# Optimization experiments

Hardware: AMD Instinct MI355X
Metric: run time of the kernel (lower is better)

## Reference

```python
import jax, jax.numpy as jnp
import numpy as np

C = 512      # input/value channels
DK = 64      # key/query channels (C // 8, SAGAN convention)
N = 4096     # flattened spatial positions (64x64)


def setup_inputs() -> dict:
    key = jax.random.key(0)
    k1, k2, k3, k4 = jax.random.split(key, 4)
    x = jax.random.normal(k1, (C, N), dtype=jnp.float32)
    # 1x1 conv projections == linear maps over the channel dim
    Wk = jax.random.normal(k2, (DK, C), dtype=jnp.float32) * (1.0 / np.sqrt(C))
    Wq = jax.random.normal(k3, (DK, C), dtype=jnp.float32) * (1.0 / np.sqrt(C))
    Wv = jax.random.normal(k4, (C, C), dtype=jnp.float32) * (1.0 / np.sqrt(C))
    return {"x": x, "Wk": Wk, "Wq": Wq, "Wv": Wv}


def reference(x, Wk, Wq, Wv):
    # conv 1x1 projections: [dk, N] / [dk, N] / [C, N]
    kx = Wk @ x
    qx = Wq @ x
    vx = Wv @ x
    # alpha_{i,j} = softmax_j( f(x_i)^T g(x_j) )  -> [N, N]
    scores = jnp.einsum('di,dj->ij', kx, qx)
    attn = jax.nn.softmax(scores, axis=-1)
    # o_i = sum_j alpha_{i,j} h(x_j)  -> [N, C]
    out = attn @ vx.T
    return out
```

## Files before the change

kernel.cpp:

```cpp
#include <hip/hip_runtime.h>
#include <hip/hip_bf16.h>

typedef __bf16 bf16x8 __attribute__((ext_vector_type(8)));
typedef float f32x4 __attribute__((ext_vector_type(4)));
typedef unsigned int u32x4 __attribute__((ext_vector_type(4)));

#define MFMA16(a, b, c) __builtin_amdgcn_mfma_f32_16x16x32_bf16((a), (b), (c), 0, 0, 0)
#define DEVI static __device__ __forceinline__

DEVI unsigned short f2bf(float f) {
  union { float f; unsigned u; } x; x.f = f;
  unsigned r = x.u + 0x7fffu + ((x.u >> 16) & 1u);
  return (unsigned short)(r >> 16);
}
DEVI float bf2f(unsigned short h) {
  union { unsigned u; float f; } x; x.u = ((unsigned)h) << 16;
  return x.f;
}
DEVI bf16x8 ld16(const void* p) {
  u32x4 t = *reinterpret_cast<const u32x4*>(p);
  return __builtin_bit_cast(bf16x8, t);
}

__global__ __launch_bounds__(256) void xsplit_kernel(const float* __restrict__ x,
    unsigned short* __restrict__ xThi, unsigned short* __restrict__ xTlo) {
  __shared__ unsigned short hs[64][72];
  __shared__ unsigned short ls[64][72];
  const int c0 = blockIdx.x * 64, j0 = blockIdx.y * 64;
  const int t = threadIdx.x;
  {
    const int cr = t >> 2, jc = (t & 3) * 16;
    const float4* s4 = reinterpret_cast<const float4*>(x + (c0 + cr) * 4096 + j0 + jc);
#pragma unroll
    for (int q = 0; q < 4; ++q) {
      float4 v = s4[q];
      float vv[4] = {v.x, v.y, v.z, v.w};
#pragma unroll
      for (int e = 0; e < 4; ++e) {
        unsigned short h = f2bf(vv[e]);
        hs[cr][jc + q * 4 + e] = h;
        ls[cr][jc + q * 4 + e] = f2bf(vv[e] - bf2f(h));
      }
    }
  }
  __syncthreads();
  {
    const int jr = t >> 2, cc = (t & 3) * 16;
    unsigned short hb[16] __attribute__((aligned(16)));
    unsigned short lb[16] __attribute__((aligned(16)));
#pragma unroll
    for (int u = 0; u < 16; ++u) { hb[u] = hs[cc + u][jr]; lb[u] = ls[cc + u][jr]; }
    unsigned short* dh = xThi + (j0 + jr) * 512 + c0 + cc;
    unsigned short* dl = xTlo + (j0 + jr) * 512 + c0 + cc;
    reinterpret_cast<u32x4*>(dh)[0] = reinterpret_cast<const u32x4*>(hb)[0];
    reinterpret_cast<u32x4*>(dh)[1] = reinterpret_cast<const u32x4*>(hb)[1];
    reinterpret_cast<u32x4*>(dl)[0] = reinterpret_cast<const u32x4*>(lb)[0];
    reinterpret_cast<u32x4*>(dl)[1] = reinterpret_cast<const u32x4*>(lb)[1];
  }
}

__global__ __launch_bounds__(256) void wsplit_all_kernel(
    const float* __restrict__ Wk, const float* __restrict__ Wq, const float* __restrict__ Wv,
    unsigned short* __restrict__ Wkhi, unsigned short* __restrict__ Wklo,
    unsigned short* __restrict__ Wqhi, unsigned short* __restrict__ Wqlo,
    unsigned short* __restrict__ Wvhi, unsigned short* __restrict__ Wvlo) {
  const int nk = 64 * 512 / 4, nv = 512 * 512 / 4;
  int i = blockIdx.x * 256 + threadIdx.x;
  const float* in; unsigned short* hi; unsigned short* lo; int idx;
  if (i < nk)            { in = Wk; hi = Wkhi; lo = Wklo; idx = i; }
  else if (i < 2 * nk)   { in = Wq; hi = Wqhi; lo = Wqlo; idx = i - nk; }
  else if (i < 2 * nk + nv) { in = Wv; hi = Wvhi; lo = Wvlo; idx = i - 2 * nk; }
  else return;
  float4 v = reinterpret_cast<const float4*>(in)[idx];
  float vv[4] = {v.x, v.y, v.z, v.w};
  unsigned short hb[4] __attribute__((aligned(8)));
  unsigned short lb[4] __attribute__((aligned(8)));
#pragma unroll
  for (int e = 0; e < 4; ++e) { hb[e] = f2bf(vv[e]); lb[e] = f2bf(vv[e] - bf2f(hb[e])); }
  reinterpret_cast<uint2*>(hi)[idx] = *reinterpret_cast<const uint2*>(hb);
  reinterpret_cast<uint2*>(lo)[idx] = *reinterpret_cast<const uint2*>(lb);
}

__global__ __launch_bounds__(256) void kqproj_kernel(
    const unsigned short* __restrict__ Wkhi, const unsigned short* __restrict__ Wklo,
    const unsigned short* __restrict__ Wqhi, const unsigned short* __restrict__ Wqlo,
    const unsigned short* __restrict__ xThi, const unsigned short* __restrict__ xTlo,
    unsigned short* __restrict__ kxThi, unsigned short* __restrict__ kxTlo,
    unsigned short* __restrict__ qxThi, unsigned short* __restrict__ qxTlo) {
  const int mb = blockIdx.y;
  const int w = threadIdx.x >> 6, lane = threadIdx.x & 63;
  const int li = lane & 15, g = lane >> 4;
  const int j0 = blockIdx.x * 64 + w * 16;
  const unsigned short* Whi = (mb < 4 ? Wkhi : Wqhi) + ((mb & 3) * 16 + li) * 512 + g * 8;
  const unsigned short* Wlo = (mb < 4 ? Wklo : Wqlo) + ((mb & 3) * 16 + li) * 512 + g * 8;
  const unsigned short* Xh = xThi + (j0 + li) * 512 + g * 8;
  const unsigned short* Xl = xTlo + (j0 + li) * 512 + g * 8;
  f32x4 acc = f32x4{0.f, 0.f, 0.f, 0.f};
  for (int kf = 0; kf < 16; ++kf) {
    const int o = kf * 32;
    bf16x8 ah = ld16(Whi + o), al = ld16(Wlo + o);
    bf16x8 bh = ld16(Xh + o), bl = ld16(Xl + o);
    acc = MFMA16(ah, bh, acc);
    acc = MFMA16(ah, bl, acc);
    acc = MFMA16(al, bh, acc);
  }
  unsigned short hv[4] __attribute__((aligned(8))), lv[4] __attribute__((aligned(8)));
#pragma unroll
  for (int r = 0; r < 4; ++r) {
    hv[r] = f2bf(acc[r]);
    lv[r] = f2bf(acc[r] - bf2f(hv[r]));
  }
  unsigned short* oh = (mb < 4 ? kxThi : qxThi) + (j0 + li) * 64 + (mb & 3) * 16 + g * 4;
  unsigned short* ol = (mb < 4 ? kxTlo : qxTlo) + (j0 + li) * 64 + (mb & 3) * 16 + g * 4;
  *reinterpret_cast<uint2*>(oh) = *reinterpret_cast<const uint2*>(hv);
  *reinterpret_cast<uint2*>(ol) = *reinterpret_cast<const uint2*>(lv);
}

__global__ __launch_bounds__(256) void vproj_kernel(
    const unsigned short* __restrict__ Wvhi, const unsigned short* __restrict__ Wvlo,
    const unsigned short* __restrict__ xThi, const unsigned short* __restrict__ xTlo,
    unsigned short* __restrict__ vbf) {
  const int w = threadIdx.x >> 6, lane = threadIdx.x & 63;
  const int li = lane & 15, g = lane >> 4;
  const int j0 = blockIdx.x * 64 + (w >> 1) * 32;
  const int c0 = blockIdx.y * 64 + (w & 1) * 32;
  f32x4 acc[2][2];
#pragma unroll
  for (int mf = 0; mf < 2; ++mf)
#pragma unroll
    for (int nf = 0; nf < 2; ++nf) acc[mf][nf] = f32x4{0.f, 0.f, 0.f, 0.f};
  for (int kf = 0; kf < 16; ++kf) {
    const int kk = kf * 32 + g * 8;
    bf16x8 ah[2], al[2], bh[2], bl[2];
#pragma unroll
    for (int mf = 0; mf < 2; ++mf) {
      ah[mf] = ld16(xThi + (j0 + mf * 16 + li) * 512 + kk);
      al[mf] = ld16(xTlo + (j0 + mf * 16 + li) * 512 + kk);
    }
#pragma unroll
    for (int nf = 0; nf < 2; ++nf) {
      bh[nf] = ld16(Wvhi + (c0 + nf * 16 + li) * 512 + kk);
      bl[nf] = ld16(Wvlo + (c0 + nf * 16 + li) * 512 + kk);
    }
#pragma unroll
    for (int mf = 0; mf < 2; ++mf)
#pragma unroll
      for (int nf = 0; nf < 2; ++nf) {
        acc[mf][nf] = MFMA16(ah[mf], bh[nf], acc[mf][nf]);
        acc[mf][nf] = MFMA16(ah[mf], bl[nf], acc[mf][nf]);
        acc[mf][nf] = MFMA16(al[mf], bh[nf], acc[mf][nf]);
      }
  }
#pragma unroll
  for (int mf = 0; mf < 2; ++mf)
#pragma unroll
    for (int nf = 0; nf < 2; ++nf) {
      unsigned short hv[4] __attribute__((aligned(8)));
#pragma unroll
      for (int r = 0; r < 4; ++r) hv[r] = f2bf(acc[mf][nf][r]);
      *reinterpret_cast<uint2*>(vbf + (size_t)(c0 + nf * 16 + li) * 4096 + j0 + mf * 16 + g * 4) =
          *reinterpret_cast<const uint2*>(hv);
    }
}

__global__ __launch_bounds__(256, 2) void attn_kernel(
    const unsigned short* __restrict__ kxThi, const unsigned short* __restrict__ kxTlo,
    const unsigned short* __restrict__ qxThi, const unsigned short* __restrict__ qxTlo,
    const unsigned short* __restrict__ vbf,
    unsigned short* __restrict__ pacc, float* __restrict__ pml, int split) {
  __shared__ __align__(16) unsigned short QLh[4096];
  __shared__ __align__(16) unsigned short QLl[4096];
  __shared__ __align__(16) unsigned short PL[4096];
  __shared__ __align__(16) float smax[64][4];
  __shared__ __align__(16) float ssum[64][4];
  const int jchunk = 4096 / split;
  const int s = blockIdx.x % split;
  const int i0 = (blockIdx.x / split) * 64;
  const int jbase = s * jchunk;
  const int w = threadIdx.x >> 6, lane = threadIdx.x & 63;
  const int li = lane & 15, g = lane >> 4;
  const float L2E = 1.4426950408889634f;
  char* qlh = reinterpret_cast<char*>(QLh);
  char* qll = reinterpret_cast<char*>(QLl);
  char* plb = reinterpret_cast<char*>(PL);

  {
    const int qi = threadIdx.x >> 2;
#pragma unroll
    for (int cc = 0; cc < 2; ++cc) {
      const int ch = (threadIdx.x & 3) + cc * 4;
      const int src = (i0 + qi) * 64 + ch * 8;
      const int dst = (qi * 128 + ch * 16) ^ ((qi & 7) << 4);
      *reinterpret_cast<u32x4*>(qlh + dst) = *reinterpret_cast<const u32x4*>(kxThi + src);
      *reinterpret_cast<u32x4*>(qll + dst) = *reinterpret_cast<const u32x4*>(kxTlo + src);
    }
  }
  f32x4 acc[8][4];
#pragma unroll
  for (int cf = 0; cf < 8; ++cf)
#pragma unroll
    for (int f = 0; f < 4; ++f) acc[cf][f] = f32x4{0.f, 0.f, 0.f, 0.f};
  float m_run[4] = {-3.0e38f, -3.0e38f, -3.0e38f, -3.0e38f};
  float l_run[4] = {0.f, 0.f, 0.f, 0.f};
  __syncthreads();

  for (int jj = 0; jj < jchunk; jj += 64) {
    const int j0 = jbase + jj;
    f32x4 sc[4];
#pragma unroll
    for (int f = 0; f < 4; ++f) sc[f] = f32x4{0.f, 0.f, 0.f, 0.f};
    {
      const unsigned short* ah_p = qxThi + (j0 + w * 16 + li) * 64 + g * 8;
      const unsigned short* al_p = qxTlo + (j0 + w * 16 + li) * 64 + g * 8;
#pragma unroll
      for (int kf = 0; kf < 2; ++kf) {
        bf16x8 ah = ld16(ah_p + kf * 32);
        bf16x8 al = ld16(al_p + kf * 32);
#pragma unroll
        for (int f = 0; f < 4; ++f) {
          const int qb = ((f * 16 + li) * 128 + kf * 64 + g * 16) ^ ((li & 7) << 4);
          bf16x8 qh = ld16(qlh + qb);
          bf16x8 ql = ld16(qll + qb);
          sc[f] = MFMA16(ah, qh, sc[f]);
          sc[f] = MFMA16(ah, ql, sc[f]);
          sc[f] = MFMA16(al, qh, sc[f]);
        }
      }
    }
    {
      float pm[4];
#pragma unroll
      for (int f = 0; f < 4; ++f) {
        float t = fmaxf(fmaxf(sc[f][0], sc[f][1]), fmaxf(sc[f][2], sc[f][3]));
        t = fmaxf(t, __shfl_xor(t, 16));
        t = fmaxf(t, __shfl_xor(t, 32));
        pm[f] = t;
      }
      if (lane < 16) {
#pragma unroll
        for (int f = 0; f < 4; ++f) smax[f * 16 + li][w] = pm[f];
      }
    }
    __syncthreads();
    float m_new[4], fac[4];
#pragma unroll
    for (int f = 0; f < 4; ++f) {
      const f32x4 sm = *reinterpret_cast<const f32x4*>(&smax[f * 16 + li][0]);
      m_new[f] = fmaxf(m_run[f], fmaxf(fmaxf(sm[0], sm[1]), fmaxf(sm[2], sm[3])));
      fac[f] = exp2f((m_run[f] - m_new[f]) * L2E);
      m_run[f] = m_new[f];
    }
#pragma unroll
    for (int f = 0; f < 4; ++f) {
      float p[4];
#pragma unroll
      for (int r = 0; r < 4; ++r) p[r] = exp2f((sc[f][r] - m_new[f]) * L2E);
      float ps = (p[0] + p[1]) + (p[2] + p[3]);
      ps += __shfl_xor(ps, 16);
      ps += __shfl_xor(ps, 32);
      if (lane < 16) ssum[f * 16 + li][w] = ps;
      unsigned short pv[4] __attribute__((aligned(8)));
#pragma unroll
      for (int r = 0; r < 4; ++r) pv[r] = f2bf(p[r]);
      const int pb = ((f * 16 + li) * 128 + w * 32 + g * 8) ^ ((li & 7) << 4);
      *reinterpret_cast<uint2*>(plb + pb) = *reinterpret_cast<const uint2*>(pv);
    }
    __syncthreads();
#pragma unroll
    for (int f = 0; f < 4; ++f) {
      const f32x4 ss = *reinterpret_cast<const f32x4*>(&ssum[f * 16 + li][0]);
      l_run[f] = l_run[f] * fac[f] + ((ss[0] + ss[1]) + (ss[2] + ss[3]));
    }
#pragma unroll
    for (int cf = 0; cf < 8; ++cf)
#pragma unroll
      for (int f = 0; f < 4; ++f) {
#pragma unroll
        for (int r = 0; r < 4; ++r) acc[cf][f][r] *= fac[f];
      }
    bf16x8 bp[4][2];
#pragma unroll
    for (int f = 0; f < 4; ++f)
#pragma unroll
      for (int kf = 0; kf < 2; ++kf) {
        const int rb = ((f * 16 + li) * 128 + kf * 64 + g * 16) ^ ((li & 7) << 4);
        bp[f][kf] = ld16(plb + rb);
      }
#pragma unroll
    for (int cf = 0; cf < 8; ++cf) {
      const unsigned short* vp = vbf + (size_t)(w * 128 + cf * 16 + li) * 4096 + j0 + g * 8;
      bf16x8 a0 = ld16(vp);
      bf16x8 a1 = ld16(vp + 32);
#pragma unroll
      for (int f = 0; f < 4; ++f) {
        acc[cf][f] = MFMA16(a0, bp[f][0], acc[cf][f]);
        acc[cf][f] = MFMA16(a1, bp[f][1], acc[cf][f]);
      }
    }
  }
#pragma unroll
  for (int cf = 0; cf < 8; ++cf)
#pragma unroll
    for (int f = 0; f < 4; ++f) {
      unsigned short hv[4] __attribute__((aligned(8)));
#pragma unroll
      for (int r = 0; r < 4; ++r) hv[r] = f2bf(acc[cf][f][r]);
      unsigned short* dp = pacc + ((size_t)(s * 4096 + i0 + f * 16 + li)) * 512 + w * 128 + cf * 16 + g * 4;
      *reinterpret_cast<uint2*>(dp) = *reinterpret_cast<const uint2*>(hv);
    }
  if (w == 0 && lane < 16) {
#pragma unroll
    for (int f = 0; f < 4; ++f) {
      pml[((size_t)(s * 4096 + i0 + f * 16 + li)) * 2] = m_run[f];
      pml[((size_t)(s * 4096 + i0 + f * 16 + li)) * 2 + 1] = l_run[f];
    }
  }
}

__global__ __launch_bounds__(256) void combine_kernel(
    const unsigned short* __restrict__ pacc, const float* __restrict__ pml,
    float* __restrict__ out, int split) {
  const int t = blockIdx.x * 256 + threadIdx.x;
  const int i = t >> 6, c8 = (t & 63) << 3;
  const float L2E = 1.4426950408889634f;
  float M = -3.0e38f;
  for (int ss = 0; ss < split; ++ss) M = fmaxf(M, pml[((size_t)ss * 4096 + i) * 2]);
  float num[8];
#pragma unroll
  for (int e = 0; e < 8; ++e) num[e] = 0.f;
  float den = 0.f;
  for (int ss = 0; ss < split; ++ss) {
    const float m = pml[((size_t)ss * 4096 + i) * 2];
    const float l = pml[((size_t)ss * 4096 + i) * 2 + 1];
    const float wgt = exp2f((m - M) * L2E);
    den += wgt * l;
    u32x4 pk = *reinterpret_cast<const u32x4*>(pacc + ((size_t)ss * 4096 + i) * 512 + c8);
#pragma unroll
    for (int e = 0; e < 8; ++e) {
      unsigned short h = (unsigned short)((pk[e >> 1] >> ((e & 1) * 16)) & 0xffffu);
      num[e] += wgt * bf2f(h);
    }
  }
  const float inv = 1.0f / den;
  float4 o0, o1;
  o0.x = num[0] * inv; o0.y = num[1] * inv; o0.z = num[2] * inv; o0.w = num[3] * inv;
  o1.x = num[4] * inv; o1.y = num[5] * inv; o1.z = num[6] * inv; o1.w = num[7] * inv;
  float* op = out + (size_t)i * 512 + c8;
  *reinterpret_cast<float4*>(op) = o0;
  *reinterpret_cast<float4*>(op + 4) = o1;
}

extern "C" void kernel_launch(void* const* d_in, const int* in_sizes, int n_in,
                              void* d_out, int out_size, void* d_ws, size_t ws_size,
                              hipStream_t stream) {
  const float* x  = (const float*)d_in[0];
  const float* Wk = (const float*)d_in[1];
  const float* Wq = (const float*)d_in[2];
  const float* Wv = (const float*)d_in[3];
  float* out = (float*)d_out;
  char* ws = (char*)d_ws;

  const size_t MB = 1024ull * 1024ull;
  const size_t pers_b = 2 * MB  + 4 * MB ;
  int split = 8;
  {
    size_t need8 = (size_t)8 * 4 * MB + 8 * 4096 * 8 + pers_b;
    if (ws_size < need8) split = 4;
  }
  const size_t pacc_b = (size_t)split * 4 * MB;
  const size_t pml_b  = (size_t)split * 4096 * 8;

  char* pers = ws + pacc_b + pml_b;
  unsigned short* pacc  = (unsigned short*)ws;
  float*          pml   = (float*)(ws + pacc_b);
  unsigned short* kxThi = (unsigned short*)(pers + 0 * 512 * 1024);
  unsigned short* kxTlo = (unsigned short*)(pers + 1 * 512 * 1024);
  unsigned short* qxThi = (unsigned short*)(pers + 2 * 512 * 1024);
  unsigned short* qxTlo = (unsigned short*)(pers + 3 * 512 * 1024);
  unsigned short* vbf   = (unsigned short*)(pers + 4 * 512 * 1024);
  unsigned short* xThi = (unsigned short*)(ws + 0 * MB);
  unsigned short* xTlo = (unsigned short*)(ws + 4 * MB);
  char* wbase = ws + 8 * MB;
  unsigned short* Wkhi = (unsigned short*)(wbase + 0 * 64 * 1024);
  unsigned short* Wklo = (unsigned short*)(wbase + 1 * 64 * 1024);
  unsigned short* Wqhi = (unsigned short*)(wbase + 2 * 64 * 1024);
  unsigned short* Wqlo = (unsigned short*)(wbase + 3 * 64 * 1024);
  unsigned short* Wvhi = (unsigned short*)(wbase + 4 * 64 * 1024);
  unsigned short* Wvlo = (unsigned short*)(wbase + 12 * 64 * 1024);
  (void)in_sizes; (void)n_in; (void)out_size;

  hipLaunchKernelGGL(xsplit_kernel, dim3(8, 64), dim3(256), 0, stream, x, xThi, xTlo);
  hipLaunchKernelGGL(wsplit_all_kernel, dim3(320), dim3(256), 0, stream,
                     Wk, Wq, Wv, Wkhi, Wklo, Wqhi, Wqlo, Wvhi, Wvlo);
  hipLaunchKernelGGL(kqproj_kernel, dim3(64, 8), dim3(256), 0, stream,
                     Wkhi, Wklo, Wqhi, Wqlo, xThi, xTlo, kxThi, kxTlo, qxThi, qxTlo);
  hipLaunchKernelGGL(vproj_kernel, dim3(64, 8), dim3(256), 0, stream, Wvhi, Wvlo, xThi, xTlo, vbf);
  hipLaunchKernelGGL(attn_kernel, dim3(64 * split), dim3(256), 0, stream,
                     kxThi, kxTlo, qxThi, qxTlo, vbf, pacc, pml, split);
  hipLaunchKernelGGL(combine_kernel, dim3(1024), dim3(256), 0, stream, pacc, pml, out, split);
}
```

Measured before the change: 175.6 us.

## Merge prep and projection kernels, keep Q in registers, lazy softmax rescale

Folds the x-split and weight-split kernels into one launch and the K/Q and V projection kernels into another, cutting the launch count from six to four. In the attention kernel, the Q fragments now stay in registers instead of being staged through LDS, which removes the shared-memory copy and a barrier. The online softmax only raises the running max, and rescales the accumulators, when the new block max exceeds the old one by more than 8. This skips most of the per-iteration rescale multiplies, but lets exp values grow up to about e^8 before the bf16 cast, and the extra registers may hurt occupancy.

```diff
diff --git a/kernel.cpp b/kernel.cpp
--- a/kernel.cpp
+++ b/kernel.cpp
@@ -22,145 +22,146 @@
   return __builtin_bit_cast(bf16x8, t);
 }
 
-__global__ __launch_bounds__(256) void xsplit_kernel(const float* __restrict__ x,
-    unsigned short* __restrict__ xThi, unsigned short* __restrict__ xTlo) {
-  __shared__ unsigned short hs[64][72];
-  __shared__ unsigned short ls[64][72];
-  const int c0 = blockIdx.x * 64, j0 = blockIdx.y * 64;
-  const int t = threadIdx.x;
-  {
-    const int cr = t >> 2, jc = (t & 3) * 16;
-    const float4* s4 = reinterpret_cast<const float4*>(x + (c0 + cr) * 4096 + j0 + jc);
-#pragma unroll
-    for (int q = 0; q < 4; ++q) {
-      float4 v = s4[q];
-      float vv[4] = {v.x, v.y, v.z, v.w};
-#pragma unroll
-      for (int e = 0; e < 4; ++e) {
-        unsigned short h = f2bf(vv[e]);
-        hs[cr][jc + q * 4 + e] = h;
-        ls[cr][jc + q * 4 + e] = f2bf(vv[e] - bf2f(h));
-      }
-    }
-  }
-  __syncthreads();
-  {
-    const int jr = t >> 2, cc = (t & 3) * 16;
-    unsigned short hb[16] __attribute__((aligned(16)));
-    unsigned short lb[16] __attribute__((aligned(16)));
-#pragma unroll
-    for (int u = 0; u < 16; ++u) { hb[u] = hs[cc + u][jr]; lb[u] = ls[cc + u][jr]; }
-    unsigned short* dh = xThi + (j0 + jr) * 512 + c0 + cc;
-    unsigned short* dl = xTlo + (j0 + jr) * 512 + c0 + cc;
-    reinterpret_cast<u32x4*>(dh)[0] = reinterpret_cast<const u32x4*>(hb)[0];
-    reinterpret_cast<u32x4*>(dh)[1] = reinterpret_cast<const u32x4*>(hb)[1];
-    reinterpret_cast<u32x4*>(dl)[0] = reinterpret_cast<const u32x4*>(lb)[0];
-    reinterpret_cast<u32x4*>(dl)[1] = reinterpret_cast<const u32x4*>(lb)[1];
-  }
-}
-
-__global__ __launch_bounds__(256) void wsplit_all_kernel(
+__global__ __launch_bounds__(256) void prep_kernel(
+    const float* __restrict__ x,
     const float* __restrict__ Wk, const float* __restrict__ Wq, const float* __restrict__ Wv,
+    unsigned short* __restrict__ xThi, unsigned short* __restrict__ xTlo,
     unsigned short* __restrict__ Wkhi, unsigned short* __restrict__ Wklo,
     unsigned short* __restrict__ Wqhi, unsigned short* __restrict__ Wqlo,
     unsigned short* __restrict__ Wvhi, unsigned short* __restrict__ Wvlo) {
-  const int nk = 64 * 512 / 4, nv = 512 * 512 / 4;
-  int i = blockIdx.x * 256 + threadIdx.x;
-  const float* in; unsigned short* hi; unsigned short* lo; int idx;
-  if (i < nk)            { in = Wk; hi = Wkhi; lo = Wklo; idx = i; }
-  else if (i < 2 * nk)   { in = Wq; hi = Wqhi; lo = Wqlo; idx = i - nk; }
-  else if (i < 2 * nk + nv) { in = Wv; hi = Wvhi; lo = Wvlo; idx = i - 2 * nk; }
-  else return;
-  float4 v = reinterpret_cast<const float4*>(in)[idx];
-  float vv[4] = {v.x, v.y, v.z, v.w};
-  unsigned short hb[4] __attribute__((aligned(8)));
-  unsigned short lb[4] __attribute__((aligned(8)));
-#pragma unroll
-  for (int e = 0; e < 4; ++e) { hb[e] = f2bf(vv[e]); lb[e] = f2bf(vv[e] - bf2f(hb[e])); }
-  reinterpret_cast<uint2*>(hi)[idx] = *reinterpret_cast<const uint2*>(hb);
-  reinterpret_cast<uint2*>(lo)[idx] = *reinterpret_cast<const uint2*>(lb);
-}
-
-__global__ __launch_bounds__(256) void kqproj_kernel(
+  __shared__ float xs[64][65];
+  const int bid = blockIdx.x;
+  const int t = threadIdx.x;
+  if (bid < 512) {
+    const int c0 = (bid & 7) * 64, j0 = (bid >> 3) * 64;
+    {
+      const int cr = t >> 2, jc = (t & 3) * 16;
+      const float4* s4 = reinterpret_cast<const float4*>(x + (size_t)(c0 + cr) * 4096 + j0 + jc);
+#pragma unroll
+      for (int q = 0; q < 4; ++q) {
+        float4 v = s4[q];
+        xs[cr][jc + q * 4 + 0] = v.x;
+        xs[cr][jc + q * 4 + 1] = v.y;
+        xs[cr][jc + q * 4 + 2] = v.z;
+        xs[cr][jc + q * 4 + 3] = v.w;
+      }
+    }
+    __syncthreads();
+    {
+      const int jr = t >> 2, cs = (t & 3) * 16;
+      unsigned short hb[16] __attribute__((aligned(16)));
+      unsigned short lb[16] __attribute__((aligned(16)));
+#pragma unroll
+      for (int u = 0; u < 16; ++u) {
+        float v = xs[cs + u][jr];
+        unsigned short h = f2bf(v);
+        hb[u] = h;
+        lb[u] = f2bf(v - bf2f(h));
+      }
+      unsigned short* dh = xThi + (size_t)(j0 + jr) * 512 + c0 + cs;
+      unsigned short* dl = xTlo + (size_t)(j0 + jr) * 512 + c0 + cs;
+      reinterpret_cast<u32x4*>(dh)[0] = reinterpret_cast<const u32x4*>(hb)[0];
+      reinterpret_cast<u32x4*>(dh)[1] = reinterpret_cast<const u32x4*>(hb)[1];
+      reinterpret_cast<u32x4*>(dl)[0] = reinterpret_cast<const u32x4*>(lb)[0];
+      reinterpret_cast<u32x4*>(dl)[1] = reinterpret_cast<const u32x4*>(lb)[1];
+    }
+  } else {
+    const int nk = 64 * 512 / 4, nv = 512 * 512 / 4;
+    int i = (bid - 512) * 256 + t;
+    const float* in; unsigned short* hi; unsigned short* lo; int idx;
+    if (i < nk)               { in = Wk; hi = Wkhi; lo = Wklo; idx = i; }
+    else if (i < 2 * nk)      { in = Wq; hi = Wqhi; lo = Wqlo; idx = i - nk; }
+    else if (i < 2 * nk + nv) { in = Wv; hi = Wvhi; lo = Wvlo; idx = i - 2 * nk; }
+    else return;
+    float4 v = reinterpret_cast<const float4*>(in)[idx];
+    float vv[4] = {v.x, v.y, v.z, v.w};
+    unsigned short hb[4] __attribute__((aligned(8)));
+    unsigned short lb[4] __attribute__((aligned(8)));
+#pragma unroll
+    for (int e = 0; e < 4; ++e) { hb[e] = f2bf(vv[e]); lb[e] = f2bf(vv[e] - bf2f(hb[e])); }
+    reinterpret_cast<uint2*>(hi)[idx] = *reinterpret_cast<const uint2*>(hb);
+    reinterpret_cast<uint2*>(lo)[idx] = *reinterpret_cast<const uint2*>(lb);
+  }
+}
+
+__global__ __launch_bounds__(256) void proj_kernel(
     const unsigned short* __restrict__ Wkhi, const unsigned short* __restrict__ Wklo,
     const unsigned short* __restrict__ Wqhi, const unsigned short* __restrict__ Wqlo,
+    const unsigned short* __restrict__ Wvhi, const unsigned short* __restrict__ Wvlo,
     const unsigned short* __restrict__ xThi, const unsigned short* __restrict__ xTlo,
     unsigned short* __restrict__ kxThi, unsigned short* __restrict__ kxTlo,
-    unsigned short* __restrict__ qxThi, unsigned short* __restrict__ qxTlo) {
-  const int mb = blockIdx.y;
+    unsigned short* __restrict__ qxThi, unsigned short* __restrict__ qxTlo,
+    unsigned short* __restrict__ vbf) {
+  const int y = blockIdx.y;
   const int w = threadIdx.x >> 6, lane = threadIdx.x & 63;
   const int li = lane & 15, g = lane >> 4;
-  const int j0 = blockIdx.x * 64 + w * 16;
-  const unsigned short* Whi = (mb < 4 ? Wkhi : Wqhi) + ((mb & 3) * 16 + li) * 512 + g * 8;
-  const unsigned short* Wlo = (mb < 4 ? Wklo : Wqlo) + ((mb & 3) * 16 + li) * 512 + g * 8;
-  const unsigned short* Xh = xThi + (j0 + li) * 512 + g * 8;
-  const unsigned short* Xl = xTlo + (j0 + li) * 512 + g * 8;
-  f32x4 acc = f32x4{0.f, 0.f, 0.f, 0.f};
-  for (int kf = 0; kf < 16; ++kf) {
-    const int o = kf * 32;
-    bf16x8 ah = ld16(Whi + o), al = ld16(Wlo + o);
-    bf16x8 bh = ld16(Xh + o), bl = ld16(Xl + o);
-    acc = MFMA16(ah, bh, acc);
-    acc = MFMA16(ah, bl, acc);
-    acc = MFMA16(al, bh, acc);
-  }
-  unsigned short hv[4] __attribute__((aligned(8))), lv[4] __attribute__((aligned(8)));
-#pragma unroll
-  for (int r = 0; r < 4; ++r) {
-    hv[r] = f2bf(acc[r]);
-    lv[r] = f2bf(acc[r] - bf2f(hv[r]));
-  }
-  unsigned short* oh = (mb < 4 ? kxThi : qxThi) + (j0 + li) * 64 + (mb & 3) * 16 + g * 4;
-  unsigned short* ol = (mb < 4 ? kxTlo : qxTlo) + (j0 + li) * 64 + (mb & 3) * 16 + g * 4;
-  *reinterpret_cast<uint2*>(oh) = *reinterpret_cast<const uint2*>(hv);
-  *reinterpret_cast<uint2*>(ol) = *reinterpret_cast<const uint2*>(lv);
-}
-
-__global__ __launch_bounds__(256) void vproj_kernel(
-    const unsigned short* __restrict__ Wvhi, const unsigned short* __restrict__ Wvlo,
-    const unsigned short* __restrict__ xThi, const unsigned short* __restrict__ xTlo,
-    unsigned short* __restrict__ vbf) {
-  const int w = threadIdx.x >> 6, lane = threadIdx.x & 63;
-  const int li = lane & 15, g = lane >> 4;
-  const int j0 = blockIdx.x * 64 + (w >> 1) * 32;
-  const int c0 = blockIdx.y * 64 + (w & 1) * 32;
-  f32x4 acc[2][2];
-#pragma unroll
-  for (int mf = 0; mf < 2; ++mf)
-#pragma unroll
-    for (int nf = 0; nf < 2; ++nf) acc[mf][nf] = f32x4{0.f, 0.f, 0.f, 0.f};
-  for (int kf = 0; kf < 16; ++kf) {
-    const int kk = kf * 32 + g * 8;
-    bf16x8 ah[2], al[2], bh[2], bl[2];
-#pragma unroll
-    for (int mf = 0; mf < 2; ++mf) {
-      ah[mf] = ld16(xThi + (j0 + mf * 16 + li) * 512 + kk);
-      al[mf] = ld16(xTlo + (j0 + mf * 16 + li) * 512 + kk);
-    }
-#pragma unroll
-    for (int nf = 0; nf < 2; ++nf) {
-      bh[nf] = ld16(Wvhi + (c0 + nf * 16 + li) * 512 + kk);
-      bl[nf] = ld16(Wvlo + (c0 + nf * 16 + li) * 512 + kk);
-    }
+  if (y < 8) {
+    const int j0 = blockIdx.x * 64 + (w >> 1) * 32;
+    const int c0 = y * 64 + (w & 1) * 32;
+    f32x4 acc[2][2];
 #pragma unroll
     for (int mf = 0; mf < 2; ++mf)
 #pragma unroll
+      for (int nf = 0; nf < 2; ++nf) acc[mf][nf] = f32x4{0.f, 0.f, 0.f, 0.f};
+    for (int kf = 0; kf < 16; ++kf) {
+      const int kk = kf * 32 + g * 8;
+      bf16x8 ah[2], al[2], bh[2], bl[2];
+#pragma unroll
+      for (int mf = 0; mf < 2; ++mf) {
+        ah[mf] = ld16(xThi + (size_t)(j0 + mf * 16 + li) * 512 + kk);
+        al[mf] = ld16(xTlo + (size_t)(j0 + mf * 16 + li) * 512 + kk);
+      }
+#pragma unroll
       for (int nf = 0; nf < 2; ++nf) {
-        acc[mf][nf] = MFMA16(ah[mf], bh[nf], acc[mf][nf]);
-        acc[mf][nf] = MFMA16(ah[mf], bl[nf], acc[mf][nf]);
-        acc[mf][nf] = MFMA16(al[mf], bh[nf], acc[mf][nf]);
-      }
-  }
-#pragma unroll
-  for (int mf = 0; mf < 2; ++mf)
-#pragma unroll
-    for (int nf = 0; nf < 2; ++nf) {
-      unsigned short hv[4] __attribute__((aligned(8)));
-#pragma unroll
-      for (int r = 0; r < 4; ++r) hv[r] = f2bf(acc[mf][nf][r]);
-      *reinterpret_cast<uint2*>(vbf + (size_t)(c0 + nf * 16 + li) * 4096 + j0 + mf * 16 + g * 4) =
-          *reinterpret_cast<const uint2*>(hv);
-    }
+        bh[nf] = ld16(Wvhi + (size_t)(c0 + nf * 16 + li) * 512 + kk);
+        bl[nf] = ld16(Wvlo + (size_t)(c0 + nf * 16 + li) * 512 + kk);
+      }
+#pragma unroll
+      for (int mf = 0; mf < 2; ++mf)
+#pragma unroll
+        for (int nf = 0; nf < 2; ++nf) {
+          acc[mf][nf] = MFMA16(ah[mf], bh[nf], acc[mf][nf]);
+          acc[mf][nf] = MFMA16(ah[mf], bl[nf], acc[mf][nf]);
+          acc[mf][nf] = MFMA16(al[mf], bh[nf], acc[mf][nf]);
+        }
+    }
+#pragma unroll
+    for (int mf = 0; mf < 2; ++mf)
+#pragma unroll
+      for (int nf = 0; nf < 2; ++nf) {
+        unsigned short hv[4] __attribute__((aligned(8)));
+#pragma unroll
+        for (int r = 0; r < 4; ++r) hv[r] = f2bf(acc[mf][nf][r]);
+        *reinterpret_cast<uint2*>(vbf + (size_t)(c0 + nf * 16 + li) * 4096 + j0 + mf * 16 + g * 4) =
+            *reinterpret_cast<const uint2*>(hv);
+      }
+  } else {
+    const int mb = y - 8;
+    const int j0 = blockIdx.x * 64 + w * 16;
+    const unsigned short* Whi = (mb < 4 ? Wkhi : Wqhi) + (size_t)((mb & 3) * 16 + li) * 512 + g * 8;
+    const unsigned short* Wlo = (mb < 4 ? Wklo : Wqlo) + (size_t)((mb & 3) * 16 + li) * 512 + g * 8;
+    const unsigned short* Xh = xThi + (size_t)(j0 + li) * 512 + g * 8;
+    const unsigned short* Xl = xTlo + (size_t)(j0 + li) * 512 + g * 8;
+    f32x4 acc = f32x4{0.f, 0.f, 0.f, 0.f};
+    for (int kf = 0; kf < 16; ++kf) {
+      const int o = kf * 32;
+      bf16x8 ah = ld16(Whi + o), al = ld16(Wlo + o);
+      bf16x8 bh = ld16(Xh + o), bl = ld16(Xl + o);
+      acc = MFMA16(ah, bh, acc);
+      acc = MFMA16(ah, bl, acc);
+      acc = MFMA16(al, bh, acc);
+    }
+    unsigned short hv[4] __attribute__((aligned(8))), lv[4] __attribute__((aligned(8)));
+#pragma unroll
+    for (int r = 0; r < 4; ++r) {
+      hv[r] = f2bf(acc[r]);
+      lv[r] = f2bf(acc[r] - bf2f(hv[r]));
+    }
+    unsigned short* oh = (mb < 4 ? kxThi : qxThi) + (size_t)(j0 + li) * 64 + (mb & 3) * 16 + g * 4;
+    unsigned short* ol = (mb < 4 ? kxTlo : qxTlo) + (size_t)(j0 + li) * 64 + (mb & 3) * 16 + g * 4;
+    *reinterpret_cast<uint2*>(oh) = *reinterpret_cast<const uint2*>(hv);
+    *reinterpret_cast<uint2*>(ol) = *reinterpret_cast<const uint2*>(lv);
+  }
 }
 
 __global__ __launch_bounds__(256, 2) void attn_kernel(
@@ -168,8 +169,6 @@
     const unsigned short* __restrict__ qxThi, const unsigned short* __restrict__ qxTlo,
     const unsigned short* __restrict__ vbf,
     unsigned short* __restrict__ pacc, float* __restrict__ pml, int split) {
-  __shared__ __align__(16) unsigned short QLh[4096];
-  __shared__ __align__(16) unsigned short QLl[4096];
   __shared__ __align__(16) unsigned short PL[4096];
   __shared__ __align__(16) float smax[64][4];
   __shared__ __align__(16) float ssum[64][4];
@@ -180,21 +179,17 @@
   const int w = threadIdx.x >> 6, lane = threadIdx.x & 63;
   const int li = lane & 15, g = lane >> 4;
   const float L2E = 1.4426950408889634f;
-  char* qlh = reinterpret_cast<char*>(QLh);
-  char* qll = reinterpret_cast<char*>(QLl);
   char* plb = reinterpret_cast<char*>(PL);
 
-  {
-    const int qi = threadIdx.x >> 2;
-#pragma unroll
-    for (int cc = 0; cc < 2; ++cc) {
-      const int ch = (threadIdx.x & 3) + cc * 4;
-      const int src = (i0 + qi) * 64 + ch * 8;
-      const int dst = (qi * 128 + ch * 16) ^ ((qi & 7) << 4);
-      *reinterpret_cast<u32x4*>(qlh + dst) = *reinterpret_cast<const u32x4*>(kxThi + src);
-      *reinterpret_cast<u32x4*>(qll + dst) = *reinterpret_cast<const u32x4*>(kxTlo + src);
-    }
-  }
+  bf16x8 qh[4][2], ql[4][2];
+#pragma unroll
+  for (int f = 0; f < 4; ++f)
+#pragma unroll
+    for (int kf = 0; kf < 2; ++kf) {
+      const size_t o = (size_t)(i0 + f * 16 + li) * 64 + kf * 32 + g * 8;
+      qh[f][kf] = ld16(kxThi + o);
+      ql[f][kf] = ld16(kxTlo + o);
+    }
   f32x4 acc[8][4];
 #pragma unroll
   for (int cf = 0; cf < 8; ++cf)
@@ -202,7 +197,6 @@
     for (int f = 0; f < 4; ++f) acc[cf][f] = f32x4{0.f, 0.f, 0.f, 0.f};
   float m_run[4] = {-3.0e38f, -3.0e38f, -3.0e38f, -3.0e38f};
   float l_run[4] = {0.f, 0.f, 0.f, 0.f};
-  __syncthreads();
 
   for (int jj = 0; jj < jchunk; jj += 64) {
     const int j0 = jbase + jj;
@@ -210,20 +204,17 @@
 #pragma unroll
     for (int f = 0; f < 4; ++f) sc[f] = f32x4{0.f, 0.f, 0.f, 0.f};
     {
-      const unsigned short* ah_p = qxThi + (j0 + w * 16 + li) * 64 + g * 8;
-      const unsigned short* al_p = qxTlo + (j0 + w * 16 + li) * 64 + g * 8;
+      const unsigned short* ah_p = qxThi + (size_t)(j0 + w * 16 + li) * 64 + g * 8;
+      const unsigned short* al_p = qxTlo + (size_t)(j0 + w * 16 + li) * 64 + g * 8;
 #pragma unroll
       for (int kf = 0; kf < 2; ++kf) {
         bf16x8 ah = ld16(ah_p + kf * 32);
         bf16x8 al = ld16(al_p + kf * 32);
 #pragma unroll
         for (int f = 0; f < 4; ++f) {
-          const int qb = ((f * 16 + li) * 128 + kf * 64 + g * 16) ^ ((li & 7) << 4);
-          bf16x8 qh = ld16(qlh + qb);
-          bf16x8 ql = ld16(qll + qb);
-          sc[f] = MFMA16(ah, qh, sc[f]);
-          sc[f] = MFMA16(ah, ql, sc[f]);
-          sc[f] = MFMA16(al, qh, sc[f]);
+          sc[f] = MFMA16(ah, qh[f][kf], sc[f]);
+          sc[f] = MFMA16(ah, ql[f][kf], sc[f]);
+          sc[f] = MFMA16(al, qh[f][kf], sc[f]);
         }
       }
     }
@@ -231,10 +222,10 @@
       float pm[4];
 #pragma unroll
       for (int f = 0; f < 4; ++f) {
-        float t = fmaxf(fmaxf(sc[f][0], sc[f][1]), fmaxf(sc[f][2], sc[f][3]));
-        t = fmaxf(t, __shfl_xor(t, 16));
-        t = fmaxf(t, __shfl_xor(t, 32));
-        pm[f] = t;
+        float tm = fmaxf(fmaxf(sc[f][0], sc[f][1]), fmaxf(sc[f][2], sc[f][3]));
+        tm = fmaxf(tm, __shfl_xor(tm, 16));
+        tm = fmaxf(tm, __shfl_xor(tm, 32));
+        pm[f] = tm;
       }
       if (lane < 16) {
 #pragma unroll
@@ -242,19 +233,27 @@
       }
     }
     __syncthreads();
-    float m_new[4], fac[4];
+    float fac[4];
 #pragma unroll
     for (int f = 0; f < 4; ++f) {
       const f32x4 sm = *reinterpret_cast<const f32x4*>(&smax[f * 16 + li][0]);
-      m_new[f] = fmaxf(m_run[f], fmaxf(fmaxf(sm[0], sm[1]), fmaxf(sm[2], sm[3])));
-      fac[f] = exp2f((m_run[f] - m_new[f]) * L2E);
-      m_run[f] = m_new[f];
+      const float m_new = fmaxf(fmaxf(sm[0], sm[1]), fmaxf(sm[2], sm[3]));
+      fac[f] = 1.0f;
+      if (m_new > m_run[f] + 8.0f) {
+        fac[f] = exp2f((m_run[f] - m_new) * L2E);
+        m_run[f] = m_new;
+#pragma unroll
+        for (int cf = 0; cf < 8; ++cf) {
+#pragma unroll
+          for (int r = 0; r < 4; ++r) acc[cf][f][r] *= fac[f];
+        }
+      }
     }
 #pragma unroll
     for (int f = 0; f < 4; ++f) {
       float p[4];
 #pragma unroll
-      for (int r = 0; r < 4; ++r) p[r] = exp2f((sc[f][r] - m_new[f]) * L2E);
+      for (int r = 0; r < 4; ++r) p[r] = exp2f((sc[f][r] - m_run[f]) * L2E);
       float ps = (p[0] + p[1]) + (p[2] + p[3]);
       ps += __shfl_xor(ps, 16);
       ps += __shfl_xor(ps, 32);
@@ -271,13 +270,6 @@
       const f32x4 ss = *reinterpret_cast<const f32x4*>(&ssum[f * 16 + li][0]);
       l_run[f] = l_run[f] * fac[f] + ((ss[0] + ss[1]) + (ss[2] + ss[3]));
     }
-#pragma unroll
-    for (int cf = 0; cf < 8; ++cf)
-#pragma unroll
-      for (int f = 0; f < 4; ++f) {
-#pragma unroll
-        for (int r = 0; r < 4; ++r) acc[cf][f][r] *= fac[f];
-      }
     bf16x8 bp[4][2];
 #pragma unroll
     for (int f = 0; f < 4; ++f)
@@ -389,12 +381,11 @@
   unsigned short* Wvlo = (unsigned short*)(wbase + 12 * 64 * 1024);
   (void)in_sizes; (void)n_in; (void)out_size;
 
-  hipLaunchKernelGGL(xsplit_kernel, dim3(8, 64), dim3(256), 0, stream, x, xThi, xTlo);
-  hipLaunchKernelGGL(wsplit_all_kernel, dim3(320), dim3(256), 0, stream,
-                     Wk, Wq, Wv, Wkhi, Wklo, Wqhi, Wqlo, Wvhi, Wvlo);
-  hipLaunchKernelGGL(kqproj_kernel, dim3(64, 8), dim3(256), 0, stream,
-                     Wkhi, Wklo, Wqhi, Wqlo, xThi, xTlo, kxThi, kxTlo, qxThi, qxTlo);
-  hipLaunchKernelGGL(vproj_kernel, dim3(64, 8), dim3(256), 0, stream, Wvhi, Wvlo, xThi, xTlo, vbf);
+  hipLaunchKernelGGL(prep_kernel, dim3(512 + 320), dim3(256), 0, stream,
+                     x, Wk, Wq, Wv, xThi, xTlo, Wkhi, Wklo, Wqhi, Wqlo, Wvhi, Wvlo);
+  hipLaunchKernelGGL(proj_kernel, dim3(64, 16), dim3(256), 0, stream,
+                     Wkhi, Wklo, Wqhi, Wqlo, Wvhi, Wvlo, xThi, xTlo,
+                     kxThi, kxTlo, qxThi, qxTlo, vbf);
   hipLaunchKernelGGL(attn_kernel, dim3(64 * split), dim3(256), 0, stream,
                      kxThi, kxTlo, qxThi, qxTlo, vbf, pacc, pml, split);
   hipLaunchKernelGGL(combine_kernel, dim3(1024), dim3(256), 0, stream, pacc, pml, out, split);
```

Result: slower. 188.2 us (+7.1%).
